# Kernel tuning notes

Hardware: AMD Instinct MI355X
Metric: run time of the kernel (lower is better)

The kernel has to match this reference:

```python
import jax, jax.numpy as jnp
import numpy as np

N_NODES = 100000


def setup_inputs() -> dict:
    key = jax.random.key(0)
    ks = jax.random.split(key, 10)
    N, T, IN, H, OUT = N_NODES, 20, 1, 64, 1
    E = 3200000
    s = 1.0 / np.sqrt(H)
    return {
        "x": jax.random.normal(ks[0], (N, T, IN), dtype=jnp.float32),
        "edge_index": jax.random.randint(ks[1], (E, 2), 0, N, dtype=jnp.int64),
        "W_ih": jax.random.uniform(ks[2], (H, IN), jnp.float32, -s, s),
        "b_ih": jax.random.uniform(ks[3], (H,), jnp.float32, -s, s),
        "W_hh": jax.random.uniform(ks[4], (H, H), jnp.float32, -s, s),
        "b_hh": jax.random.uniform(ks[5], (H,), jnp.float32, -s, s),
        "W_gcn": jax.random.uniform(ks[6], (H, H), jnp.float32, -s, s),
        "b_gcn": jax.random.uniform(ks[7], (H,), jnp.float32, -s, s),
        "W_fc": jax.random.uniform(ks[8], (OUT, H), jnp.float32, -s, s),
        "b_fc": jax.random.uniform(ks[9], (OUT,), jnp.float32, -s, s),
    }


def _strnn_fwd(x, edge_index, W_ih, b_ih, W_hh, b_hh, W_gcn, b_gcn, W_fc, b_fc):
    N = x.shape[0]
    H = W_hh.shape[0]

    # ---- vanilla tanh RNN (batch_first); only last hidden state is needed ----
    xs = jnp.swapaxes(x, 0, 1)  # [T, N, in]

    def step(h, xt):
        h = jnp.tanh(xt @ W_ih.T + b_ih + h @ W_hh.T + b_hh)
        return h, None

    h_last, _ = jax.lax.scan(step, jnp.zeros((N, H), x.dtype), xs)  # [N, H]

    # ---- GCNConv: add self-loops, sym-normalize, linear, scatter-add ----
    src = edge_index[:, 0]
    dst = edge_index[:, 1]
    loop = jnp.arange(N, dtype=src.dtype)
    src = jnp.concatenate([src, loop])
    dst = jnp.concatenate([dst, loop])

    xw = h_last @ W_gcn.T  # [N, H]
    deg = jax.ops.segment_sum(jnp.ones_like(dst, dtype=xw.dtype), dst, num_segments=N)
    dinv = jnp.where(deg > 0, jax.lax.rsqrt(deg), 0.0)
    norm = dinv[src] * dinv[dst]  # [E+N]

    msgs = xw[src] * norm[:, None]  # gather + scale, [E+N, H]
    agg = jax.ops.segment_sum(msgs, dst, num_segments=N) + b_gcn  # scatter-add

    return agg @ W_fc.T + b_fc  # [N, out]


def reference(x, edge_index, W_ih, b_ih, W_hh, b_hh, W_gcn, b_gcn, W_fc, b_fc):
    return _strnn_fwd(x, edge_index, W_ih, b_ih, W_hh, b_hh, W_gcn, b_gcn, W_fc, b_fc)
```

## Files before the change

### kernel.cpp

```cpp
#include <hip/hip_runtime.h>

#define TT 20
#define HH 64
#define RSZ 32768
#define DRSZ 32768
#define NSL 64
#define NSLD 32

typedef __attribute__((ext_vector_type(8))) short short8;
typedef __attribute__((ext_vector_type(4))) float f32x4;

__device__ __forceinline__ unsigned fbits(float f) { union { float f; unsigned u; } v; v.f = f; return v.u; }
__device__ __forceinline__ float bcast(unsigned u) { union { float f; unsigned u; } v; v.u = u; return v.f; }

__global__ __launch_bounds__(256, 3) void k_fused(
    const float* __restrict__ x,
    const float* __restrict__ W_ih, const float* __restrict__ b_ih,
    const float* __restrict__ W_hh, const float* __restrict__ b_hh,
    const float* __restrict__ W_gcn, const float* __restrict__ W_fc,
    const int* __restrict__ ei, unsigned* __restrict__ degrep,
    float* __restrict__ z, int N, int E, int RD, int N4)
{
    __shared__ __align__(16) unsigned smem[8192];

    const int t = threadIdx.x;
    const int RDN = RD * NSLD;

    if (blockIdx.x < RDN) {
        unsigned* bin = smem;
        const int r = blockIdx.x % RD;
        const int s = blockIdx.x / RD;
        const int base = r * DRSZ;
        for (int i = t; i < DRSZ / 4; i += 256) bin[i] = 0;
        __syncthreads();
        const long long P = (long long)(E >> 1);
        const long long pb = s * P / NSLD;
        const long long pe = (s + 1) * P / NSLD;
        const int4* ei4 = (const int4*)ei;
        for (long long g = pb + t; g < pe; g += 256) {
            int4 q = ei4[g];
            unsigned u0 = (unsigned)(q.y - base);
            unsigned u1 = (unsigned)(q.w - base);
            if (u0 < DRSZ) atomicAdd(&bin[u0 >> 2], 1u << ((u0 & 3) << 3));
            if (u1 < DRSZ) atomicAdd(&bin[u1 >> 2], 1u << ((u1 & 3) << 3));
        }
        if ((E & 1) && s == NSLD - 1 && t == 0) {
            unsigned u = (unsigned)(ei[2 * (E - 1) + 1] - base);
            if (u < DRSZ) atomicAdd(&bin[u >> 2], 1u << ((u & 3) << 3));
        }
        __syncthreads();
        const int lim = min(DRSZ, N - base);
        const int words = (lim + 3) >> 2;
        unsigned* dst = degrep + (size_t)s * N4 + (base >> 2);
        for (int i = t; i < words; i += 256) dst[i] = bin[i];
        return;
    }

    const int w    = t >> 6;
    const int l    = t & 63;
    const int nl   = l & 15;
    const int quad = l >> 4;
    const int n0   = (blockIdx.x - RDN) * 64 + w * 16;

    unsigned short* hh = (unsigned short*)&smem[w * 512];
    unsigned short* hl = (unsigned short*)&smem[2048 + w * 512];
    float*          sx = (float*)&smem[4096 + w * 320];

    for (int i = l; i < 16 * TT; i += 64) {
        int nn = i / TT, tt = i - nn * TT;
        int n = n0 + nn; if (n >= N) n = N - 1;
        sx[tt * 16 + nn] = x[(size_t)n * TT + tt];
    }
    {
        uint4 zz = {0, 0, 0, 0};
        uint4* ph = (uint4*)hh;
        uint4* pl = (uint4*)hl;
#pragma unroll
        for (int i = 0; i < 2; ++i) { ph[l + 64 * i] = zz; pl[l + 64 * i] = zz; }
    }

    short8 Bh[4][2], Bl[4][2];
#pragma unroll
    for (int tt2 = 0; tt2 < 4; ++tt2)
#pragma unroll
        for (int kc = 0; kc < 2; ++kc) {
            const float* wr = W_hh + (size_t)(16 * tt2 + nl) * HH + kc * 32 + quad * 8;
            float4 w0 = *(const float4*)(wr);
            float4 w1 = *(const float4*)(wr + 4);
            float wvv[8] = {w0.x, w0.y, w0.z, w0.w, w1.x, w1.y, w1.z, w1.w};
            short8 sh, sl;
#pragma unroll
            for (int j = 0; j < 8; ++j) {
                unsigned u  = fbits(wvv[j]);
                unsigned hb = u & 0xffff0000u;
                float lo = wvv[j] - bcast(hb);
                sh[j] = (short)(hb >> 16);
                sl[j] = (short)(fbits(lo) >> 16);
            }
            Bh[tt2][kc] = sh; Bl[tt2][kc] = sl;
        }

    float vl = 0.0f;
#pragma unroll 8
    for (int j = 0; j < HH; ++j) vl = fmaf(W_fc[j], W_gcn[j * HH + l], vl);

    float wih4[4], bs4[4], vv[4];
#pragma unroll
    for (int tt2 = 0; tt2 < 4; ++tt2) {
        int n = nl + 16 * tt2;
        wih4[tt2] = W_ih[n];
        bs4[tt2]  = b_ih[n] + b_hh[n];
        vv[tt2]   = __shfl(vl, n, 64);
    }

    const int ra = (l ^ ((l >> 4) & 1)) * 8;

    f32x4 C[4];

    for (int step = 0; step < TT; ++step) {
        const float4 xr = *(const float4*)&sx[step * 16 + quad * 4];
#pragma unroll
        for (int tt2 = 0; tt2 < 4; ++tt2) {
            C[tt2][0] = fmaf(xr.x, wih4[tt2], bs4[tt2]);
            C[tt2][1] = fmaf(xr.y, wih4[tt2], bs4[tt2]);
            C[tt2][2] = fmaf(xr.z, wih4[tt2], bs4[tt2]);
            C[tt2][3] = fmaf(xr.w, wih4[tt2], bs4[tt2]);
        }

#pragma unroll
        for (int kc = 0; kc < 2; ++kc) {
            short8 Ah = *(const short8*)&hh[kc * 512 + ra];
            short8 Al = *(const short8*)&hl[kc * 512 + ra];
#pragma unroll
            for (int tt2 = 0; tt2 < 4; ++tt2) {
                C[tt2] = __builtin_amdgcn_mfma_f32_16x16x32_bf16(Ah, Bh[tt2][kc], C[tt2], 0, 0, 0);
                C[tt2] = __builtin_amdgcn_mfma_f32_16x16x32_bf16(Ah, Bl[tt2][kc], C[tt2], 0, 0, 0);
                C[tt2] = __builtin_amdgcn_mfma_f32_16x16x32_bf16(Al, Bh[tt2][kc], C[tt2], 0, 0, 0);
            }
        }

#pragma unroll
        for (int tt2 = 0; tt2 < 4; ++tt2) {
            const int kc_d = tt2 >> 1;
            const int qa   = (nl >> 3) + 2 * (tt2 & 1);
            const int jj   = nl & 7;
#pragma unroll
            for (int r = 0; r < 4; ++r) {
                float eg = __builtin_amdgcn_exp2f(C[tt2][r] * 2.885390081777927f);
                float hv = fmaf(-2.0f, __builtin_amdgcn_rcpf(eg + 1.0f), 1.0f);
                C[tt2][r] = hv;
                unsigned um = fbits(hv);
                unsigned hb = um & 0xffff0000u;
                float lo = hv - bcast(hb);
                const int m   = quad * 4 + r;
                const int la  = m + 16 * qa;
                const int idx = kc_d * 512 + (la ^ ((la >> 4) & 1)) * 8 + jj;
                hh[idx] = (unsigned short)(um >> 16);
                hl[idx] = (unsigned short)(fbits(lo) >> 16);
            }
        }
    }

#pragma unroll
    for (int r = 0; r < 4; ++r) {
        float p = 0.0f;
#pragma unroll
        for (int tt2 = 0; tt2 < 4; ++tt2) p = fmaf(C[tt2][r], vv[tt2], p);
        p += __shfl_xor(p, 1, 64);
        p += __shfl_xor(p, 2, 64);
        p += __shfl_xor(p, 4, 64);
        p += __shfl_xor(p, 8, 64);
        if (nl == 0) {
            const int n = n0 + quad * 4 + r;
            if (n < N) z[n] = p;
        }
    }
}

__global__ __launch_bounds__(256) void k_w(const unsigned* __restrict__ degrep,
                                           const float* __restrict__ z,
                                           float* __restrict__ dinv,
                                           float* __restrict__ w, int N, int N4) {
    int n = blockIdx.x * blockDim.x + threadIdx.x;
    if (n >= N) return;
    const int wd = n >> 2, sh = (n & 3) << 3;
    unsigned d = 0;
#pragma unroll 8
    for (int s = 0; s < NSLD; ++s) d += (degrep[(size_t)s * N4 + wd] >> sh) & 0xffu;
    float di = __frsqrt_rn((float)d + 1.0f);
    dinv[n] = di;
    w[n] = di * z[n];
}

__global__ __launch_bounds__(1024) void k_edge_bin(const int* __restrict__ ei,
                                                   const float* __restrict__ w,
                                                   float* __restrict__ Srep,
                                                   int N, int E, int R) {
    extern __shared__ float bin[];
    const int r = blockIdx.x % R;
    const int s = blockIdx.x / R;
    const int base = r * RSZ;
    for (int i = threadIdx.x; i < RSZ; i += 1024) bin[i] = 0.0f;
    __syncthreads();
    const long long P = (long long)(E >> 1);
    const long long pb = s * P / NSL;
    const long long pe = (s + 1) * P / NSL;
    const int4* ei4 = (const int4*)ei;
    for (long long g = pb + threadIdx.x; g < pe; g += 1024) {
        int4 q = ei4[g];
        unsigned u0 = (unsigned)(q.y - base);
        unsigned u1 = (unsigned)(q.w - base);
        if (u0 < RSZ) atomicAdd(&bin[u0], w[q.x]);
        if (u1 < RSZ) atomicAdd(&bin[u1], w[q.z]);
    }
    if ((E & 1) && s == NSL - 1 && threadIdx.x == 0) {
        unsigned u = (unsigned)(ei[2 * (E - 1) + 1] - base);
        if (u < RSZ) atomicAdd(&bin[u], w[ei[2 * (E - 1)]]);
    }
    __syncthreads();
    const int lim = min(RSZ, N - base);
    float* dst = Srep + (size_t)s * N + base;
    for (int i = threadIdx.x; i < lim; i += 1024) dst[i] = bin[i];
}

__global__ __launch_bounds__(256) void k_final(const float* __restrict__ dinv,
                                               const float* __restrict__ Srep,
                                               const float* __restrict__ w,
                                               const float* __restrict__ b_gcn,
                                               const float* __restrict__ W_fc,
                                               const float* __restrict__ b_fc,
                                               float* __restrict__ out, int N)
{
    float c = b_fc[0];
#pragma unroll 8
    for (int j = 0; j < HH; ++j) c = fmaf(W_fc[j], b_gcn[j], c);
    int n = blockIdx.x * blockDim.x + threadIdx.x;
    if (n >= N) return;
    float S = 0.0f;
#pragma unroll 8
    for (int s = 0; s < NSL; ++s) S += Srep[(size_t)s * N + n];
    float d = dinv[n];
    out[n] = fmaf(d, S, fmaf(d, w[n], c));
}

extern "C" void kernel_launch(void* const* d_in, const int* in_sizes, int n_in,
                              void* d_out, int out_size, void* d_ws, size_t ws_size,
                              hipStream_t stream)
{
    const float* x     = (const float*)d_in[0];
    const int*   ei    = (const int*)d_in[1];
    const float* W_ih  = (const float*)d_in[2];
    const float* b_ih  = (const float*)d_in[3];
    const float* W_hh  = (const float*)d_in[4];
    const float* b_hh  = (const float*)d_in[5];
    const float* W_gcn = (const float*)d_in[6];
    const float* b_gcn = (const float*)d_in[7];
    const float* W_fc  = (const float*)d_in[8];
    const float* b_fc  = (const float*)d_in[9];
    float* out = (float*)d_out;

    const int N  = in_sizes[0] / TT;
    const int E  = in_sizes[1] / 2;
    const int N4 = (N + 3) / 4;
    const int RD = (N + DRSZ - 1) / DRSZ;
    const int RS = (N + RSZ - 1) / RSZ;

    static bool s_attr = false;
    if (!s_attr) {
        hipFuncSetAttribute((const void*)k_edge_bin,
                            hipFuncAttributeMaxDynamicSharedMemorySize, RSZ * 4);
        s_attr = true;
    }

    char* ws = (char*)d_ws;
    size_t off = 0;
    auto alloc = [&](size_t bytes) { void* p = ws + off; off += (bytes + 255) & ~(size_t)255; return p; };
    unsigned* degrep = (unsigned*)alloc((size_t)NSLD * N4 * 4);
    float*    Srep   = (float*)   alloc((size_t)NSL * N * 4);
    float*    z      = (float*)   alloc((size_t)N * 4);
    float*    dinv   = (float*)   alloc((size_t)N * 4);
    float*    w      = (float*)   alloc((size_t)N * 4);

    const int rnnBlocks = (N + 63) / 64;
    k_fused   <<<RD * NSLD + rnnBlocks, 256, 0, stream>>>(x, W_ih, b_ih, W_hh, b_hh,
                                                          W_gcn, W_fc, ei, degrep,
                                                          z, N, E, RD, N4);
    k_w       <<<(N + 255) / 256, 256, 0, stream>>>(degrep, z, dinv, w, N, N4);
    k_edge_bin<<<RS * NSL, 1024, RSZ * 4, stream>>>(ei, w, Srep, N, E, RS);
    k_final   <<<(N + 255) / 256, 256, 0, stream>>>(dinv, Srep, w, b_gcn, W_fc, b_fc, out, N);
}
```

Measured before the change: 215.9 us.

## Transpose RNN MFMA so hidden state stays in registers, removing LDS round-trip

Swaps the MFMA operand roles so W_hh is the A operand and the hidden state is the B operand. The layout trick means each step's tanh output in C registers can be repacked directly into the next step's bf16 hi/lo B fragments. This removes the per-step LDS stores and loads of the hidden state and the LDS zeroing. The input weights and biases are pre-shuffled per lane, and the final projection reduction is reorganised across quads. The cost is more registers for per-lane weight and bias copies, which could hurt occupancy.

```diff
diff --git a/kernel.cpp b/kernel.cpp
--- a/kernel.cpp
+++ b/kernel.cpp
@@ -12,6 +12,19 @@
 
 __device__ __forceinline__ unsigned fbits(float f) { union { float f; unsigned u; } v; v.f = f; return v.u; }
 __device__ __forceinline__ float bcast(unsigned u) { union { float f; unsigned u; } v; v.u = u; return v.f; }
+
+__device__ __forceinline__ unsigned pk_trunc(float a, float b) {
+    return (fbits(a) >> 16) | (fbits(b) & 0xffff0000u);
+}
+__device__ __forceinline__ unsigned pk_res(unsigned hp, float a, float b) {
+    float ra = a - bcast(hp << 16);
+    float rb = b - bcast(hp & 0xffff0000u);
+    return (fbits(ra) >> 16) | (fbits(rb) & 0xffff0000u);
+}
+union U8 { short8 s; unsigned u[4]; };
+__device__ __forceinline__ short8 mk8(unsigned a, unsigned b, unsigned c, unsigned d) {
+    U8 t; t.u[0] = a; t.u[1] = b; t.u[2] = c; t.u[3] = d; return t.s;
+}
 
 __global__ __launch_bounds__(256, 3) void k_fused(
     const float* __restrict__ x,
@@ -62,31 +75,22 @@
     const int quad = l >> 4;
     const int n0   = (blockIdx.x - RDN) * 64 + w * 16;
 
-    unsigned short* hh = (unsigned short*)&smem[w * 512];
-    unsigned short* hl = (unsigned short*)&smem[2048 + w * 512];
-    float*          sx = (float*)&smem[4096 + w * 320];
+    float* sx = (float*)&smem[w * 320];
 
     for (int i = l; i < 16 * TT; i += 64) {
         int nn = i / TT, tt = i - nn * TT;
         int n = n0 + nn; if (n >= N) n = N - 1;
         sx[tt * 16 + nn] = x[(size_t)n * TT + tt];
     }
-    {
-        uint4 zz = {0, 0, 0, 0};
-        uint4* ph = (uint4*)hh;
-        uint4* pl = (uint4*)hl;
-#pragma unroll
-        for (int i = 0; i < 2; ++i) { ph[l + 64 * i] = zz; pl[l + 64 * i] = zz; }
-    }
-
-    short8 Bh[4][2], Bl[4][2];
+
+    short8 AWh[4][2], AWl[4][2];
 #pragma unroll
     for (int tt2 = 0; tt2 < 4; ++tt2)
 #pragma unroll
         for (int kc = 0; kc < 2; ++kc) {
-            const float* wr = W_hh + (size_t)(16 * tt2 + nl) * HH + kc * 32 + quad * 8;
-            float4 w0 = *(const float4*)(wr);
-            float4 w1 = *(const float4*)(wr + 4);
+            const float* wr = W_hh + (size_t)(16 * tt2 + nl) * HH + 16 * kc + 4 * quad;
+            float4 w0 = *(const float4*)wr;
+            float4 w1 = *(const float4*)(wr + 32);
             float wvv[8] = {w0.x, w0.y, w0.z, w0.w, w1.x, w1.y, w1.z, w1.w};
             short8 sh, sl;
 #pragma unroll
@@ -97,83 +101,84 @@
                 sh[j] = (short)(hb >> 16);
                 sl[j] = (short)(fbits(lo) >> 16);
             }
-            Bh[tt2][kc] = sh; Bl[tt2][kc] = sl;
-        }
-
-    float vl = 0.0f;
-#pragma unroll 8
-    for (int j = 0; j < HH; ++j) vl = fmaf(W_fc[j], W_gcn[j * HH + l], vl);
-
-    float wih4[4], bs4[4], vv[4];
-#pragma unroll
-    for (int tt2 = 0; tt2 < 4; ++tt2) {
-        int n = nl + 16 * tt2;
-        wih4[tt2] = W_ih[n];
-        bs4[tt2]  = b_ih[n] + b_hh[n];
-        vv[tt2]   = __shfl(vl, n, 64);
-    }
-
-    const int ra = (l ^ ((l >> 4) & 1)) * 8;
+            AWh[tt2][kc] = sh; AWl[tt2][kc] = sl;
+        }
+
+    float wl_ = W_ih[l];
+    float bl_ = b_ih[l] + b_hh[l];
+    float wihf[4][4], bsf[4][4];
+#pragma unroll
+    for (int tt2 = 0; tt2 < 4; ++tt2)
+#pragma unroll
+        for (int r = 0; r < 4; ++r) {
+            int o = 16 * tt2 + 4 * quad + r;
+            wihf[tt2][r] = __shfl(wl_, o, 64);
+            bsf[tt2][r]  = __shfl(bl_, o, 64);
+        }
 
     f32x4 C[4];
+    short8 Bh[2], Bl[2];
+    Bh[0] = mk8(0, 0, 0, 0); Bh[1] = mk8(0, 0, 0, 0);
+    Bl[0] = mk8(0, 0, 0, 0); Bl[1] = mk8(0, 0, 0, 0);
 
     for (int step = 0; step < TT; ++step) {
-        const float4 xr = *(const float4*)&sx[step * 16 + quad * 4];
+        const float xv = sx[step * 16 + nl];
 #pragma unroll
         for (int tt2 = 0; tt2 < 4; ++tt2) {
-            C[tt2][0] = fmaf(xr.x, wih4[tt2], bs4[tt2]);
-            C[tt2][1] = fmaf(xr.y, wih4[tt2], bs4[tt2]);
-            C[tt2][2] = fmaf(xr.z, wih4[tt2], bs4[tt2]);
-            C[tt2][3] = fmaf(xr.w, wih4[tt2], bs4[tt2]);
-        }
-
-#pragma unroll
-        for (int kc = 0; kc < 2; ++kc) {
-            short8 Ah = *(const short8*)&hh[kc * 512 + ra];
-            short8 Al = *(const short8*)&hl[kc * 512 + ra];
+            C[tt2][0] = fmaf(xv, wihf[tt2][0], bsf[tt2][0]);
+            C[tt2][1] = fmaf(xv, wihf[tt2][1], bsf[tt2][1]);
+            C[tt2][2] = fmaf(xv, wihf[tt2][2], bsf[tt2][2]);
+            C[tt2][3] = fmaf(xv, wihf[tt2][3], bsf[tt2][3]);
+        }
+
+#pragma unroll
+        for (int kc = 0; kc < 2; ++kc)
 #pragma unroll
             for (int tt2 = 0; tt2 < 4; ++tt2) {
-                C[tt2] = __builtin_amdgcn_mfma_f32_16x16x32_bf16(Ah, Bh[tt2][kc], C[tt2], 0, 0, 0);
-                C[tt2] = __builtin_amdgcn_mfma_f32_16x16x32_bf16(Ah, Bl[tt2][kc], C[tt2], 0, 0, 0);
-                C[tt2] = __builtin_amdgcn_mfma_f32_16x16x32_bf16(Al, Bh[tt2][kc], C[tt2], 0, 0, 0);
-            }
-        }
-
-#pragma unroll
-        for (int tt2 = 0; tt2 < 4; ++tt2) {
-            const int kc_d = tt2 >> 1;
-            const int qa   = (nl >> 3) + 2 * (tt2 & 1);
-            const int jj   = nl & 7;
+                C[tt2] = __builtin_amdgcn_mfma_f32_16x16x32_bf16(AWh[tt2][kc], Bh[kc], C[tt2], 0, 0, 0);
+                C[tt2] = __builtin_amdgcn_mfma_f32_16x16x32_bf16(AWh[tt2][kc], Bl[kc], C[tt2], 0, 0, 0);
+                C[tt2] = __builtin_amdgcn_mfma_f32_16x16x32_bf16(AWl[tt2][kc], Bh[kc], C[tt2], 0, 0, 0);
+            }
+
+#pragma unroll
+        for (int tt2 = 0; tt2 < 4; ++tt2)
 #pragma unroll
             for (int r = 0; r < 4; ++r) {
                 float eg = __builtin_amdgcn_exp2f(C[tt2][r] * 2.885390081777927f);
-                float hv = fmaf(-2.0f, __builtin_amdgcn_rcpf(eg + 1.0f), 1.0f);
-                C[tt2][r] = hv;
-                unsigned um = fbits(hv);
-                unsigned hb = um & 0xffff0000u;
-                float lo = hv - bcast(hb);
-                const int m   = quad * 4 + r;
-                const int la  = m + 16 * qa;
-                const int idx = kc_d * 512 + (la ^ ((la >> 4) & 1)) * 8 + jj;
-                hh[idx] = (unsigned short)(um >> 16);
-                hl[idx] = (unsigned short)(fbits(lo) >> 16);
-            }
-        }
-    }
-
-#pragma unroll
-    for (int r = 0; r < 4; ++r) {
-        float p = 0.0f;
-#pragma unroll
-        for (int tt2 = 0; tt2 < 4; ++tt2) p = fmaf(C[tt2][r], vv[tt2], p);
-        p += __shfl_xor(p, 1, 64);
-        p += __shfl_xor(p, 2, 64);
-        p += __shfl_xor(p, 4, 64);
-        p += __shfl_xor(p, 8, 64);
-        if (nl == 0) {
-            const int n = n0 + quad * 4 + r;
-            if (n < N) z[n] = p;
-        }
+                C[tt2][r] = fmaf(-2.0f, __builtin_amdgcn_rcpf(eg + 1.0f), 1.0f);
+            }
+
+        if (step != TT - 1) {
+#pragma unroll
+            for (int kc = 0; kc < 2; ++kc) {
+                unsigned u0 = pk_trunc(C[kc][0],     C[kc][1]);
+                unsigned u1 = pk_trunc(C[kc][2],     C[kc][3]);
+                unsigned u2 = pk_trunc(C[2 + kc][0], C[2 + kc][1]);
+                unsigned u3 = pk_trunc(C[2 + kc][2], C[2 + kc][3]);
+                Bh[kc] = mk8(u0, u1, u2, u3);
+                Bl[kc] = mk8(pk_res(u0, C[kc][0],     C[kc][1]),
+                             pk_res(u1, C[kc][2],     C[kc][3]),
+                             pk_res(u2, C[2 + kc][0], C[2 + kc][1]),
+                             pk_res(u3, C[2 + kc][2], C[2 + kc][3]));
+            }
+        }
+    }
+
+    float vl = 0.0f;
+#pragma unroll 8
+    for (int j = 0; j < HH; ++j) vl = fmaf(W_fc[j], W_gcn[j * HH + l], vl);
+
+    float p = 0.0f;
+#pragma unroll
+    for (int tt2 = 0; tt2 < 4; ++tt2)
+#pragma unroll
+        for (int r = 0; r < 4; ++r)
+            p = fmaf(C[tt2][r], __shfl(vl, 16 * tt2 + 4 * quad + r, 64), p);
+    p += __shfl_xor(p, 16, 64);
+    p += __shfl_xor(p, 32, 64);
+    if (l < 16) {
+        int n = n0 + l;
+        if (n < N) z[n] = p;
     }
 }
 
```

Result: no change. 213.1 us (-1.3%).
